# Kernel optimization log

Measured on AMD Instinct MI355X. Metric: run time of the kernel, lower is better.

The kernel has to match this reference:

```python
import jax, jax.numpy as jnp
import numpy as np

TOPK_FRAC = 0.125
RMS_EPS = 1e-6


def setup_inputs() -> dict:
    key = jax.random.key(0)
    ks = jax.random.split(key, 8)
    B, S, D, DH = 8, 8192, 1024, 64
    x = jax.random.normal(ks[0], (B, S, D), dtype=jnp.float32)
    importance = jax.random.normal(ks[1], (B, S), dtype=jnp.float32)
    w_scale = 1.0 / np.sqrt(D)
    W_q = jax.random.normal(ks[2], (2 * DH, D), dtype=jnp.float32) * w_scale
    W_kv = jax.random.normal(ks[3], (3 * DH, D), dtype=jnp.float32) * w_scale
    lam_logit = jnp.float32(-0.5)
    rms_weight = jnp.ones((DH,), dtype=jnp.float32)
    merge_gate = jnp.float32(0.8)
    W_out = jax.random.normal(ks[4], (D, DH), dtype=jnp.float32) * (1.0 / np.sqrt(DH))
    b_out = jnp.zeros((D,), dtype=jnp.float32)
    return {"x": x, "importance": importance, "W_q": W_q, "W_kv": W_kv,
            "lam_logit": lam_logit, "rms_weight": rms_weight,
            "merge_gate": merge_gate, "W_out": W_out, "b_out": b_out}


def reference(x, importance, W_q, W_kv, lam_logit, rms_weight, merge_gate, W_out, b_out):
    B, S, D = x.shape
    dh = rms_weight.shape[0]
    K = max(1, int(TOPK_FRAC * S))
    # SGRSelector: top-K query positions per batch by importance
    _, top_idx = jax.lax.top_k(importance, K)            # [B, K]
    x_sel = jnp.take_along_axis(x, top_idx[:, :, None], axis=1)  # [B, K, D]
    # FusedProjectionSplit: two fused GEMMs
    q = jnp.einsum('bkd,ed->bke', x_sel, W_q)            # [B, K, 2*dh]
    kv = jnp.einsum('bsd,ed->bse', x, W_kv)              # [B, S, 3*dh]
    Q1, Q2 = q[..., :dh], q[..., dh:]
    K1, K2, V = kv[..., :dh], kv[..., dh:2 * dh], kv[..., 2 * dh:]
    scale = 1.0 / jnp.sqrt(jnp.float32(dh))
    # dual-stream differential attention (fp32, like the kernel)
    s1 = jnp.einsum('bke,bse->bks', Q1, K1) * scale
    s2 = jnp.einsum('bke,bse->bks', Q2, K2) * scale
    A1 = jax.nn.softmax(s1, axis=-1)
    A2 = jax.nn.softmax(s2, axis=-1)
    lam = jax.nn.sigmoid(lam_logit)
    attn = jnp.einsum('bks,bse->bke', A1, V) - lam * jnp.einsum('bks,bse->bke', A2, V)  # [B,K,dh]
    # RMSNorm(d_head)
    rms = jnp.sqrt(jnp.mean(attn * attn, axis=-1, keepdims=True) + RMS_EPS)
    h = attn / rms * rms_weight
    # out_proj: d_head -> d_model
    y = jnp.einsum('bke,de->bkd', h, W_out) + b_out      # [B, K, D]
    # gated merge back into the sequence at selected positions
    merged = merge_gate * y + (1.0 - merge_gate) * x_sel
    out = x.at[jnp.arange(B)[:, None], top_idx].set(merged)
    return out
```

## Files before the change

kernel.cpp:

```cpp
#include <hip/hip_runtime.h>

typedef unsigned int u32;
typedef unsigned short u16;
typedef float f32x4_t  __attribute__((ext_vector_type(4)));
typedef float f32x16_t __attribute__((ext_vector_type(16)));
typedef u32   u32x4_t  __attribute__((ext_vector_type(4)));
typedef __bf16 bf16x8_t __attribute__((ext_vector_type(8)));
typedef __bf16 bf16x2_t __attribute__((ext_vector_type(2)));

#define B_   8
#define S_   8192
#define D_   1024
#define KSEL 1024

#define OFF_WQ   0ul
#define OFF_WKV  (256ul<<10)
#define OFF_WO   (640ul<<10)
#define OFF_TIDX (768ul<<10)
#define OFF_K1   (1ul<<20)
#define OFF_K2   (OFF_K1 + (8ul<<20))
#define OFF_V    (OFF_K2 + (8ul<<20))
#define OFF_Q1   (OFF_V  + (8ul<<20))
#define OFF_Q2   (OFF_Q1 + (1ul<<20))
#define OFF_PST  (OFF_Q2 + (1ul<<20))

#define PREC 2304

static __device__ __forceinline__ u16 f2bf(float f){
  return __builtin_bit_cast(u16, (__bf16)f);
}
static __device__ __forceinline__ float bf2f(u16 v){
  u32 u = ((u32)v)<<16; return __builtin_bit_cast(float, u);
}
static __device__ __forceinline__ u32 pkbf(float a, float b){
  bf16x2_t v; v[0] = (__bf16)a; v[1] = (__bf16)b;
  return __builtin_bit_cast(u32, v);
}
static __device__ __forceinline__ f32x16_t zero16(){
  f32x16_t z;
  #pragma unroll
  for (int i=0;i<16;i++) z[i]=0.f;
  return z;
}
static __device__ __forceinline__ bf16x8_t bc8(u32x4_t v){ return __builtin_bit_cast(bf16x8_t, v); }
static __device__ __forceinline__ f32x16_t mfma32(bf16x8_t a, bf16x8_t b, f32x16_t c){
  return __builtin_amdgcn_mfma_f32_32x32x16_bf16(a,b,c,0,0,0);
}
static __device__ __forceinline__ f32x4_t mfma16(bf16x8_t a, bf16x8_t b, f32x4_t c){
  return __builtin_amdgcn_mfma_f32_16x16x32_bf16(a,b,c,0,0,0);
}
static __device__ __forceinline__ void gl_lds16(const void* g, void* l){
  __builtin_amdgcn_global_load_lds((const __attribute__((address_space(1))) u32*)g,
                                   (__attribute__((address_space(3))) u32*)l, 16, 0, 0);
}

__global__ __launch_bounds__(256) void preptopk_kernel(const float* __restrict__ wq,
                                                       const float* __restrict__ wkv,
                                                       const float* __restrict__ wo,
                                                       const float* __restrict__ imp,
                                                       u16* owq, u16* owkv, u16* owo,
                                                       int* __restrict__ tidx){
  if (blockIdx.x >= 8){
    const int i = (blockIdx.x-8)*256 + threadIdx.x;
    if (i < 128*1024) owq[i]  = f2bf(wq[i] * 0.125f);
    if (i < 192*1024) owkv[i] = f2bf(wkv[i]);
    if (i < 64*1024)  owo[i]  = f2bf(wo[i]);
    return;
  }
  const int b = blockIdx.x, t = threadIdx.x;
  __shared__ u32 hist[256];
  __shared__ u32 shPrefix;
  __shared__ int shNeed;
  __shared__ u32 cnt, eqc;
  __shared__ int eqlist[256];
  u32 key[32];
  const float* ip = imp + (long)b*S_;
  #pragma unroll
  for (int i=0;i<32;i++){
    u32 u = __builtin_bit_cast(u32, ip[t + 256*i]);
    key[i] = (u & 0x80000000u) ? ~u : (u | 0x80000000u);
  }
  if (t==0){ shPrefix = 0; shNeed = KSEL; cnt = 0; eqc = 0; }
  for (int pass=0; pass<4; ++pass){
    const int shift = 24 - 8*pass;
    __syncthreads();
    hist[t] = 0;
    __syncthreads();
    const u32 pfx = shPrefix;
    #pragma unroll
    for (int i=0;i<32;i++){
      bool act = (pass==0) || ((key[i] >> (shift+8)) == pfx);
      if (act) atomicAdd(&hist[(key[i]>>shift)&255u], 1u);
    }
    __syncthreads();
    if (t==0){
      int need = shNeed; u32 cum = 0; int c;
      for (c=255; c>=0; --c){ u32 h = hist[c]; if (cum + h >= (u32)need) break; cum += h; }
      if (c < 0) c = 0;
      shPrefix = (shPrefix<<8) | (u32)c;
      shNeed = need - (int)cum;
    }
  }
  __syncthreads();
  const u32 T = shPrefix; const int needEq = shNeed;
  #pragma unroll
  for (int i=0;i<32;i++){
    const int s = t + 256*i;
    if (key[i] > T){ u32 p = atomicAdd(&cnt,1u); tidx[b*KSEL + p] = s; }
    else if (key[i] == T){ u32 e = atomicAdd(&eqc,1u); if (e < 256u) eqlist[e] = s; }
  }
  __syncthreads();
  if (t==0){
    int n = (int)eqc; if (n > 256) n = 256;
    const int bpos = (int)cnt;
    for (int j=0;j<needEq && j<n;j++){
      int mi = j;
      for (int k2=j+1;k2<n;k2++) if (eqlist[k2] < eqlist[mi]) mi = k2;
      int tmp = eqlist[j]; eqlist[j]=eqlist[mi]; eqlist[mi]=tmp;
      tidx[b*KSEL + bpos + j] = eqlist[j];
    }
  }
}

__global__ __launch_bounds__(256,2) void kvq_kernel(const float* __restrict__ x,
                                                    const u16* __restrict__ wkv,
                                                    const u16* __restrict__ wq,
                                                    const int* __restrict__ tidx,
                                                    u16* __restrict__ K1, u16* __restrict__ K2, u16* __restrict__ V,
                                                    u16* __restrict__ Q1, u16* __restrict__ Q2,
                                                    float* __restrict__ out){
  __shared__ __align__(16) char smem[81920];
  const int tid = threadIdx.x;
  const int w = tid>>6, lane = tid&63, lo4 = lane&15, hi = lane>>4;

  if (blockIdx.x < 512){
    char* lA0 = smem;
    char* lB0 = smem + 32768;
    const long row0 = (long)blockIdx.x * 128;
    const int srow8 = tid>>4;
    const int cseg  = tid&15;
    const float* xp = x   + (row0 + srow8)*1024 + cseg*4;
    float*       op = out + (row0 + srow8)*1024 + cseg*4;
    f32x4_t acc[12][2];
    #pragma unroll
    for (int i=0;i<12;i++){ acc[i][0]=(f32x4_t){0,0,0,0}; acc[i][1]=(f32x4_t){0,0,0,0}; }
    f32x4_t f[8];

    auto LOADX = [&](int k0){
      #pragma unroll
      for (int i=0;i<8;i++) f[i] = *(const f32x4_t*)(xp + k0 + i*16*1024);
    };
    auto STORE_WRITE = [&](int k0, int buf){
      #pragma unroll
      for (int i=0;i<8;i++){
        *(f32x4_t*)(op + k0 + i*16*1024) = f[i];
        const u32 row = (u32)(srow8 + i*16);
        u32 byte = row*128u + (u32)cseg*8u;
        byte ^= (row&7u)<<4;
        uint2 p; p.x = pkbf(f[i][0], f[i][1]); p.y = pkbf(f[i][2], f[i][3]);
        *(uint2*)(lA0 + buf*16384 + byte) = p;
      }
    };
    auto STAGEB = [&](int buf, int k0){
      #pragma unroll
      for (int ii=0; ii<6; ++ii){
        const int inst = w*6 + ii;
        const u32 L = (u32)inst*1024u + (u32)lane*16u;
        const u32 n = L>>7, off = L&127u;
        const char* src = (const char*)wkv + (size_t)n*2048 + (size_t)k0*2 + (off ^ ((n&7u)<<4));
        gl_lds16(src, lB0 + buf*24576 + (size_t)inst*1024);
      }
    };

    LOADX(0); STAGEB(0, 0); STORE_WRITE(0, 0);
    __syncthreads();

    for (int t=0; t<16; ++t){
      const int cur = t&1, nxt = cur^1;
      if (t < 15){ LOADX((t+1)*64); STAGEB(nxt, (t+1)*64); }
      #pragma unroll
      for (int kk=0;kk<2;kk++){
        bf16x8_t xf[2];
        #pragma unroll
        for (int ns=0;ns<2;ns++){
          const int s = w*32 + ns*16 + lo4;
          u32 byte = ((u32)s<<7) + ((u32)kk<<6) + ((u32)hi<<4); byte ^= ((u32)(s&7))<<4;
          xf[ns] = *(const bf16x8_t*)(lA0 + cur*16384 + byte);
        }
        #pragma unroll
        for (int ms=0;ms<12;ms++){
          const int e = ms*16 + lo4;
          u32 byte = ((u32)e<<7) + ((u32)kk<<6) + ((u32)hi<<4); byte ^= ((u32)(e&7))<<4;
          const bf16x8_t wf = *(const bf16x8_t*)(lB0 + cur*24576 + byte);
          acc[ms][0] = mfma16(wf, xf[0], acc[ms][0]);
          acc[ms][1] = mfma16(wf, xf[1], acc[ms][1]);
        }
      }
      if (t < 15){ STORE_WRITE((t+1)*64, nxt); }
      __syncthreads();
    }

    #pragma unroll
    for (int ms=0;ms<12;ms++){
      const int e0 = ms*16 + 4*hi;
      const int arr = e0>>6, eh = e0&63;
      u16* basep = arr==0 ? K1 : (arr==1 ? K2 : V);
      #pragma unroll
      for (int ns=0;ns<2;ns++){
        const long srow = row0 + w*32 + ns*16 + lo4;
        ushort4 v;
        v.x = f2bf(acc[ms][ns][0]); v.y = f2bf(acc[ms][ns][1]);
        v.z = f2bf(acc[ms][ns][2]); v.w = f2bf(acc[ms][ns][3]);
        *(ushort4*)(basep + srow*64 + eh) = v;
      }
    }
  } else {
    u16* lW   = (u16*)smem;
    u16* lX   = (u16*)(smem + 16384);
    int* rows = (int*)(smem + 20480);
    const int bq = blockIdx.x - 512;
    const int b = bq >> 5, q0 = (bq & 31) * 32;
    if (tid < 32) rows[tid] = tidx[b*KSEL + q0 + tid];
    __syncthreads();
    const int sq = tid>>3, qt8 = tid&7;
    const float* xp = x + ((long)b*S_ + rows[sq])*1024 + qt8*8;
    f32x4_t acc[2][2];
    #pragma unroll
    for (int i=0;i<2;i++){ acc[i][0]=(f32x4_t){0,0,0,0}; acc[i][1]=(f32x4_t){0,0,0,0}; }

    for (int k0=0;k0<1024;k0+=64){
      __syncthreads();
      f32x4_t f0 = *(const f32x4_t*)(xp + k0);
      f32x4_t f1 = *(const f32x4_t*)(xp + k0 + 4);
      {
        const u32 byte = ((u32)sq<<7) + ((u32)(qt8 ^ (sq&7))<<4);
        *(u32x4_t*)((char*)lX + byte) =
          (u32x4_t){pkbf(f0[0],f0[1]), pkbf(f0[2],f0[3]), pkbf(f1[0],f1[1]), pkbf(f1[2],f1[3])};
      }
      #pragma unroll
      for (int ii=0; ii<4; ++ii){
        const int inst = w*4 + ii;
        const u32 L = (u32)inst*1024u + (u32)lane*16u;
        const u32 n = L>>7, off = L&127u;
        const char* src = (const char*)wq + (size_t)n*2048 + (size_t)k0*2 + (off ^ ((n&7u)<<4));
        gl_lds16(src, (char*)lW + (size_t)inst*1024);
      }
      __syncthreads();
      #pragma unroll
      for (int kk=0;kk<2;kk++){
        bf16x8_t xf[2];
        #pragma unroll
        for (int ns=0;ns<2;ns++){
          const int s = ns*16 + lo4;
          u32 byte = ((u32)s<<7) + ((u32)kk<<6) + ((u32)hi<<4); byte ^= ((u32)(s&7))<<4;
          xf[ns] = *(const bf16x8_t*)((const char*)lX + byte);
        }
        #pragma unroll
        for (int ms=0;ms<2;ms++){
          const int e = w*32 + ms*16 + lo4;
          u32 byte = ((u32)e<<7) + ((u32)kk<<6) + ((u32)hi<<4); byte ^= ((u32)(e&7))<<4;
          const bf16x8_t wf = *(const bf16x8_t*)((const char*)lW + byte);
          acc[ms][0] = mfma16(wf, xf[0], acc[ms][0]);
          acc[ms][1] = mfma16(wf, xf[1], acc[ms][1]);
        }
      }
    }
    #pragma unroll
    for (int ms=0;ms<2;ms++){
      const int e0 = w*32 + ms*16 + 4*hi;
      const int arr = e0>>6, eh = e0&63;
      u16* basep = arr ? Q2 : Q1;
      #pragma unroll
      for (int ns=0;ns<2;ns++){
        const int qg = q0 + ns*16 + lo4;
        ushort4 v;
        v.x = f2bf(acc[ms][ns][0]); v.y = f2bf(acc[ms][ns][1]);
        v.z = f2bf(acc[ms][ns][2]); v.w = f2bf(acc[ms][ns][3]);
        *(ushort4*)(basep + ((long)b*KSEL + qg)*64 + eh) = v;
      }
    }
  }
}

__global__ __launch_bounds__(256,2) void attn_kernel(
    const u16* __restrict__ Q1g, const u16* __restrict__ Q2g,
    const u16* __restrict__ K1g, const u16* __restrict__ K2g,
    const u16* __restrict__ Vg,  u16* __restrict__ pst)
{
  __shared__ __align__(16) u16 lK1[64*64];
  __shared__ __align__(16) u16 lK2[64*64];
  __shared__ __align__(16) u16 lVT[64*64];
  const int tid = threadIdx.x;
  const int w = tid>>6, lane = tid&63;
  const int lo5 = lane&31, hi = lane>>5;
  const int b  = blockIdx.x>>6;
  const int qt = (blockIdx.x>>3)&7;
  const int c  = blockIdx.x&7;
  const int qw = qt*4 + w;
  const int qg = qw*32 + lo5;

  u32x4_t qf[2][4];
  {
    const u16* q1p = Q1g + ((long)b*KSEL + qg)*64;
    const u16* q2p = Q2g + ((long)b*KSEL + qg)*64;
    #pragma unroll
    for (int ks=0;ks<4;ks++){
      qf[0][ks] = *(const u32x4_t*)(q1p + ks*16 + hi*8);
      qf[1][ks] = *(const u32x4_t*)(q2p + ks*16 + hi*8);
    }
  }
  f32x16_t O00 = zero16(), O01 = zero16(), O10 = zero16(), O11 = zero16();
  float m0v = -INFINITY, m1v = -INFINITY, l0v = 0.f, l1v = 0.f;
  const int vkey = tid&63, vdg = tid>>6;

  for (int it=0; it<16; ++it){
    const int s0 = c*1024 + it*64;
    __syncthreads();
    #pragma unroll
    for (int ii=0; ii<2; ++ii){
      const int inst = w*2 + ii;
      const u32 L = (u32)inst*1024u + (u32)lane*16u;
      const u32 r = L>>7;
      const u32 so = (r<<7) | ((L&127u) ^ ((r&7u)<<4));
      const long gb = ((long)(b*S_ + s0))*128;
      gl_lds16((const char*)K1g + gb + so, (char*)lK1 + (size_t)inst*1024);
      gl_lds16((const char*)K2g + gb + so, (char*)lK2 + (size_t)inst*1024);
    }
    {
      const u16* vp = Vg + ((long)(b*S_ + s0 + vkey))*64 + vdg*16;
      const u32x4_t va = *(const u32x4_t*)(vp);
      const u32x4_t vb = *(const u32x4_t*)(vp + 8);
      #pragma unroll
      for (int j=0;j<16;j++){
        const u32 word = (j<8) ? va[(j>>1)&3] : vb[(j>>1)&3];
        const u16 val = (u16)((j&1) ? (word>>16) : (word & 0xffffu));
        const int d = vdg*16 + j;
        u32 byte = ((u32)d<<7) + ((u32)vkey<<1);
        byte ^= ((u32)(d&7))<<4;
        *(u16*)((char*)lVT + byte) = val;
      }
    }
    __syncthreads();
    #pragma unroll
    for (int h=0; h<2; ++h){
      const u16* lK = h ? lK2 : lK1;
      f32x16_t sc0 = zero16(), sc1 = zero16();
      #pragma unroll
      for (int ks=0; ks<4; ++ks){
        u32 byteA = (((u32)lo5)<<7) + ((u32)ks<<5) + ((u32)hi<<4);
        byteA ^= ((u32)(lo5&7))<<4;
        const bf16x8_t kf0 = *(const bf16x8_t*)((const char*)lK + byteA);
        const bf16x8_t kf1 = *(const bf16x8_t*)((const char*)lK + (byteA + 4096));
        sc0 = mfma32(kf0, bc8(qf[h][ks]), sc0);
        sc1 = mfma32(kf1, bc8(qf[h][ks]), sc1);
      }
      const float mref = h ? m1v : m0v;
      float tmax = mref;
      #pragma unroll
      for (int i=0;i<16;i++){ tmax = fmaxf(tmax, sc0[i]); tmax = fmaxf(tmax, sc1[i]); }
      tmax = fmaxf(tmax, __shfl_xor(tmax, 32, 64));
      const float mnew = tmax;
      const float ce = __expf(mref - mnew);
      float lsum = 0.f;
      #pragma unroll
      for (int i=0;i<16;i++){
        sc0[i] = __expf(sc0[i]-mnew); lsum += sc0[i];
        sc1[i] = __expf(sc1[i]-mnew); lsum += sc1[i];
      }
      lsum += __shfl_xor(lsum, 32, 64);
      if (h==0){ l0v = l0v*ce + lsum; m0v = mnew; } else { l1v = l1v*ce + lsum; m1v = mnew; }
      f32x16_t &Oa = h ? O10 : O00;
      f32x16_t &Ob = h ? O11 : O01;
      #pragma unroll
      for (int i=0;i<16;i++){ Oa[i] *= ce; Ob[i] *= ce; }
      #pragma unroll
      for (int kb=0; kb<2; ++kb){
        const f32x16_t &s = kb ? sc1 : sc0;
        u32 pk[8], sx[8];
        #pragma unroll
        for (int i=0;i<8;i++) pk[i] = pkbf(s[2*i], s[2*i+1]);
        #pragma unroll
        for (int i=0;i<8;i++) sx[i] = (u32)__shfl_xor((int)pk[i], 32, 64);
        #pragma unroll
        for (int dd=0; dd<2; ++dd){
          const u32 w0 = hi ? sx[4*dd+2] : pk[4*dd];
          const u32 w1 = hi ? sx[4*dd+3] : pk[4*dd+1];
          const u32 w2 = hi ? pk[4*dd+2] : sx[4*dd];
          const u32 w3 = hi ? pk[4*dd+3] : sx[4*dd+1];
          const bf16x8_t pf = bc8((u32x4_t){w0,w1,w2,w3});
          const int ksG = kb*2 + dd;
          u32 byteV = (((u32)lo5)<<7) + ((u32)ksG<<5) + ((u32)hi<<4);
          byteV ^= ((u32)(lo5&7))<<4;
          const bf16x8_t vf0 = *(const bf16x8_t*)((const char*)lVT + byteV);
          const bf16x8_t vf1 = *(const bf16x8_t*)((const char*)lVT + (byteV + 4096));
          Oa = mfma32(vf0, pf, Oa);
          Ob = mfma32(vf1, pf, Ob);
        }
      }
    }
  }
  const long rec = (((long)b*32 + qw)*8 + c)*2;
  u16* p0 = pst + rec*PREC;
  u16* p1 = p0 + PREC;
  #pragma unroll
  for (int r2=0;r2<16;r2++){
    p0[(   r2)*64 + lane] = f2bf(O00[r2]);
    p0[(16+r2)*64 + lane] = f2bf(O01[r2]);
    p1[(   r2)*64 + lane] = f2bf(O10[r2]);
    p1[(16+r2)*64 + lane] = f2bf(O11[r2]);
  }
  ((float*)(p0+2048))[lane] = m0v; ((float*)(p0+2176))[lane] = l0v;
  ((float*)(p1+2048))[lane] = m1v; ((float*)(p1+2176))[lane] = l1v;
}

__global__ __launch_bounds__(64,1) void combine_kernel(
    const u16* __restrict__ pst, const int* __restrict__ tidx,
    const float* __restrict__ x, const float* __restrict__ rmsw,
    const float* __restrict__ lamp, const float* __restrict__ gatep,
    const u16* __restrict__ wo, const float* __restrict__ bo,
    float* __restrict__ out)
{
  const int lane = threadIdx.x, lo5 = lane&31, hi = lane>>5;
  const int sb = blockIdx.x & 3;
  const int qw = (blockIdx.x>>2) & 31;
  const int b  = blockIdx.x >> 7;
  const float lam = 1.f/(1.f + __expf(-lamp[0]));
  const float g = gatep[0];
  const long rec0 = ((long)b*32 + qw)*16;
  float att[2][16];
  #pragma unroll
  for (int h=0; h<2; ++h){
    const u16* ph = pst + (rec0 + h)*PREC;
    float mc[8], lc[8];
    float mm = -INFINITY;
    #pragma unroll
    for (int cc=0;cc<8;cc++){
      const u16* pc = ph + (size_t)cc*2*PREC;
      mc[cc] = ((const float*)(pc+2048))[lane];
      lc[cc] = ((const float*)(pc+2176))[lane];
      mm = fmaxf(mm, mc[cc]);
    }
    float ef[8]; float L = 0.f;
    #pragma unroll
    for (int cc=0;cc<8;cc++){ ef[cc] = __expf(mc[cc]-mm); L += lc[cc]*ef[cc]; }
    const float invL = 1.f/L;
    #pragma unroll
    for (int dB=0; dB<2; ++dB){
      #pragma unroll
      for (int r=0;r<16;r++){
        float o = 0.f;
        #pragma unroll
        for (int cc=0;cc<8;cc++)
          o += ef[cc]*bf2f(ph[(size_t)cc*2*PREC + (dB*16+r)*64 + lane]);
        o *= invL;
        if (h==0) att[dB][r] = o; else att[dB][r] -= lam*o;
      }
    }
  }
  float ss = 0.f;
  #pragma unroll
  for (int dB=0;dB<2;dB++)
    #pragma unroll
    for (int r=0;r<16;r++) ss += att[dB][r]*att[dB][r];
  ss += __shfl_xor(ss, 32, 64);
  const float inv = rsqrtf(ss*(1.0f/64.0f) + 1e-6f);
  #pragma unroll
  for (int dB=0;dB<2;dB++){
    #pragma unroll
    for (int rq=0;rq<4;rq++){
      const f32x4_t wv = *(const f32x4_t*)(rmsw + dB*32 + 8*rq + 4*hi);
      #pragma unroll
      for (int j=0;j<4;j++) att[dB][4*rq+j] *= inv*wv[j];
    }
  }
  bf16x8_t hf[4];
  #pragma unroll
  for (int dB=0;dB<2;dB++){
    u32 pk[8], sx[8];
    #pragma unroll
    for (int i=0;i<8;i++) pk[i] = pkbf(att[dB][2*i], att[dB][2*i+1]);
    #pragma unroll
    for (int i=0;i<8;i++) sx[i] = (u32)__shfl_xor((int)pk[i], 32, 64);
    #pragma unroll
    for (int dd=0; dd<2; ++dd){
      const u32 w0 = hi ? sx[4*dd+2] : pk[4*dd];
      const u32 w1 = hi ? sx[4*dd+3] : pk[4*dd+1];
      const u32 w2 = hi ? pk[4*dd+2] : sx[4*dd];
      const u32 w3 = hi ? pk[4*dd+3] : sx[4*dd+1];
      hf[dB*2+dd] = bc8((u32x4_t){w0,w1,w2,w3});
    }
  }
  const int srow = tidx[b*KSEL + qw*32 + lo5];
  const float* xr  = x   + ((long)b*S_ + srow)*1024;
  float*       orr = out + ((long)b*S_ + srow)*1024;
  for (int st=sb*8; st<sb*8+8; ++st){
    f32x16_t acc = zero16();
    #pragma unroll
    for (int ks=0;ks<4;ks++){
      const u32x4_t wq4 = *(const u32x4_t*)(wo + ((long)(st*32 + lo5))*64 + ks*16 + hi*8);
      acc = mfma32(bc8(wq4), hf[ks], acc);
    }
    #pragma unroll
    for (int rq=0;rq<4;rq++){
      const int d0 = st*32 + 8*rq + 4*hi;
      const f32x4_t bo4 = *(const f32x4_t*)(bo + d0);
      const f32x4_t xv  = *(const f32x4_t*)(xr + d0);
      f32x4_t mg;
      #pragma unroll
      for (int j=0;j<4;j++){
        const float y = acc[4*rq+j] + bo4[j];
        mg[j] = g*y + (1.f-g)*xv[j];
      }
      *(f32x4_t*)(orr + d0) = mg;
    }
  }
}

extern "C" void kernel_launch(void* const* d_in, const int* in_sizes, int n_in,
                              void* d_out, int out_size, void* d_ws, size_t ws_size,
                              hipStream_t stream) {
  (void)in_sizes; (void)n_in; (void)out_size; (void)ws_size;
  const float* x    = (const float*)d_in[0];
  const float* imp  = (const float*)d_in[1];
  const float* wq   = (const float*)d_in[2];
  const float* wkv  = (const float*)d_in[3];
  const float* lamp = (const float*)d_in[4];
  const float* rmsw = (const float*)d_in[5];
  const float* gate = (const float*)d_in[6];
  const float* wo   = (const float*)d_in[7];
  const float* bo   = (const float*)d_in[8];
  float* out = (float*)d_out;
  char* ws = (char*)d_ws;
  u16* Wq   = (u16*)(ws + OFF_WQ);
  u16* Wkv  = (u16*)(ws + OFF_WKV);
  u16* Wo   = (u16*)(ws + OFF_WO);
  int* Tidx = (int*)(ws + OFF_TIDX);
  u16* K1   = (u16*)(ws + OFF_K1);
  u16* K2   = (u16*)(ws + OFF_K2);
  u16* V    = (u16*)(ws + OFF_V);
  u16* Q1   = (u16*)(ws + OFF_Q1);
  u16* Q2   = (u16*)(ws + OFF_Q2);
  u16* Pst  = (u16*)(ws + OFF_PST);

  preptopk_kernel<<<776, 256, 0, stream>>>(wq, wkv, wo, imp, Wq, Wkv, Wo, Tidx);
  kvq_kernel<<<768, 256, 0, stream>>>(x, Wkv, Wq, Tidx, K1, K2, V, Q1, Q2, out);
  attn_kernel<<<512, 256, 0, stream>>>(Q1, Q2, K1, K2, V, Pst);
  combine_kernel<<<1024, 64, 0, stream>>>(Pst, Tidx, x, rmsw, lamp, gate, Wo, bo, out);
}
```

Before: 272.3 us.

## Fuse combine into attention via last-block atomic counter; lazy rescale; parallel top-k scan

Removes the separate combine kernel: each attention block writes its partial state, increments a per-(batch, query-tile) counter, and the last of the eight chunk blocks performs the merge, RMSNorm and output projection for its tile. The online softmax now rescales only when the running max grows by more than 8, skipping most exp/multiply work on the accumulators. The top-k histogram cut search is replaced by a parallel suffix scan instead of a serial loop in thread 0. The fused epilogue runs on only one block per tile with a serial 32-step output loop, which may create a tail, and the counter relies on threadfence ordering.

```diff
diff --git a/kernel.cpp b/kernel.cpp
--- a/kernel.cpp
+++ b/kernel.cpp
@@ -17,6 +17,7 @@
 #define OFF_WKV  (256ul<<10)
 #define OFF_WO   (640ul<<10)
 #define OFF_TIDX (768ul<<10)
+#define OFF_CNT  (800ul<<10)
 #define OFF_K1   (1ul<<20)
 #define OFF_K2   (OFF_K1 + (8ul<<20))
 #define OFF_V    (OFF_K2 + (8ul<<20))
@@ -59,9 +60,11 @@
                                                        const float* __restrict__ wo,
                                                        const float* __restrict__ imp,
                                                        u16* owq, u16* owkv, u16* owo,
-                                                       int* __restrict__ tidx){
+                                                       int* __restrict__ tidx,
+                                                       int* __restrict__ cnt){
   if (blockIdx.x >= 8){
     const int i = (blockIdx.x-8)*256 + threadIdx.x;
+    if (blockIdx.x == 8 && threadIdx.x < 64) cnt[threadIdx.x] = 0;
     if (i < 128*1024) owq[i]  = f2bf(wq[i] * 0.125f);
     if (i < 192*1024) owkv[i] = f2bf(wkv[i]);
     if (i < 64*1024)  owo[i]  = f2bf(wo[i]);
@@ -69,9 +72,10 @@
   }
   const int b = blockIdx.x, t = threadIdx.x;
   __shared__ u32 hist[256];
+  __shared__ u32 sscan[256];
   __shared__ u32 shPrefix;
   __shared__ int shNeed;
-  __shared__ u32 cnt, eqc;
+  __shared__ u32 cnt2, eqc;
   __shared__ int eqlist[256];
   u32 key[32];
   const float* ip = imp + (long)b*S_;
@@ -80,25 +84,34 @@
     u32 u = __builtin_bit_cast(u32, ip[t + 256*i]);
     key[i] = (u & 0x80000000u) ? ~u : (u | 0x80000000u);
   }
-  if (t==0){ shPrefix = 0; shNeed = KSEL; cnt = 0; eqc = 0; }
+  if (t==0){ shPrefix = 0; shNeed = KSEL; cnt2 = 0; eqc = 0; }
   for (int pass=0; pass<4; ++pass){
     const int shift = 24 - 8*pass;
     __syncthreads();
     hist[t] = 0;
     __syncthreads();
     const u32 pfx = shPrefix;
+    const int need = shNeed;
     #pragma unroll
     for (int i=0;i<32;i++){
       bool act = (pass==0) || ((key[i] >> (shift+8)) == pfx);
       if (act) atomicAdd(&hist[(key[i]>>shift)&255u], 1u);
     }
     __syncthreads();
-    if (t==0){
-      int need = shNeed; u32 cum = 0; int c;
-      for (c=255; c>=0; --c){ u32 h = hist[c]; if (cum + h >= (u32)need) break; cum += h; }
-      if (c < 0) c = 0;
-      shPrefix = (shPrefix<<8) | (u32)c;
-      shNeed = need - (int)cum;
+    sscan[t] = hist[t];
+    __syncthreads();
+    for (int off=1; off<256; off<<=1){
+      const u32 v = (t+off < 256) ? sscan[t+off] : 0u;
+      __syncthreads();
+      sscan[t] += v;
+      __syncthreads();
+    }
+    const u32 un = (u32)need;
+    const u32 s_t  = sscan[t];
+    const u32 s_t1 = (t<255) ? sscan[t+1] : 0u;
+    if (s_t >= un && s_t1 < un){
+      shPrefix = (pfx<<8) | (u32)t;
+      shNeed = need - (int)s_t1;
     }
   }
   __syncthreads();
@@ -106,13 +119,13 @@
   #pragma unroll
   for (int i=0;i<32;i++){
     const int s = t + 256*i;
-    if (key[i] > T){ u32 p = atomicAdd(&cnt,1u); tidx[b*KSEL + p] = s; }
+    if (key[i] > T){ u32 p = atomicAdd(&cnt2,1u); tidx[b*KSEL + p] = s; }
     else if (key[i] == T){ u32 e = atomicAdd(&eqc,1u); if (e < 256u) eqlist[e] = s; }
   }
   __syncthreads();
   if (t==0){
     int n = (int)eqc; if (n > 256) n = 256;
-    const int bpos = (int)cnt;
+    const int bpos = (int)cnt2;
     for (int j=0;j<needEq && j<n;j++){
       int mi = j;
       for (int k2=j+1;k2<n;k2++) if (eqlist[k2] < eqlist[mi]) mi = k2;
@@ -285,11 +298,17 @@
 __global__ __launch_bounds__(256,2) void attn_kernel(
     const u16* __restrict__ Q1g, const u16* __restrict__ Q2g,
     const u16* __restrict__ K1g, const u16* __restrict__ K2g,
-    const u16* __restrict__ Vg,  u16* __restrict__ pst)
+    const u16* __restrict__ Vg,  u16* __restrict__ pst,
+    int* __restrict__ cnt, const int* __restrict__ tidx,
+    const float* __restrict__ x, const float* __restrict__ rmsw,
+    const float* __restrict__ lamp, const float* __restrict__ gatep,
+    const u16* __restrict__ wo, const float* __restrict__ bo,
+    float* __restrict__ out)
 {
   __shared__ __align__(16) u16 lK1[64*64];
   __shared__ __align__(16) u16 lK2[64*64];
   __shared__ __align__(16) u16 lVT[64*64];
+  __shared__ int sOld;
   const int tid = threadIdx.x;
   const int w = tid>>6, lane = tid&63;
   const int lo5 = lane&31, hi = lane>>5;
@@ -355,12 +374,13 @@
         sc1 = mfma32(kf1, bc8(qf[h][ks]), sc1);
       }
       const float mref = h ? m1v : m0v;
-      float tmax = mref;
+      float tmax = -INFINITY;
       #pragma unroll
       for (int i=0;i<16;i++){ tmax = fmaxf(tmax, sc0[i]); tmax = fmaxf(tmax, sc1[i]); }
       tmax = fmaxf(tmax, __shfl_xor(tmax, 32, 64));
-      const float mnew = tmax;
-      const float ce = __expf(mref - mnew);
+      const bool upd = (tmax > mref + 8.f);
+      const float mnew = upd ? tmax : mref;
+      const float ce = upd ? __expf(mref - mnew) : 1.f;
       float lsum = 0.f;
       #pragma unroll
       for (int i=0;i<16;i++){
@@ -368,11 +388,14 @@
         sc1[i] = __expf(sc1[i]-mnew); lsum += sc1[i];
       }
       lsum += __shfl_xor(lsum, 32, 64);
-      if (h==0){ l0v = l0v*ce + lsum; m0v = mnew; } else { l1v = l1v*ce + lsum; m1v = mnew; }
+      if (h==0){ l0v = upd ? l0v*ce + lsum : l0v + lsum; m0v = mnew; }
+      else     { l1v = upd ? l1v*ce + lsum : l1v + lsum; m1v = mnew; }
       f32x16_t &Oa = h ? O10 : O00;
       f32x16_t &Ob = h ? O11 : O01;
-      #pragma unroll
-      for (int i=0;i<16;i++){ Oa[i] *= ce; Ob[i] *= ce; }
+      if (upd){
+        #pragma unroll
+        for (int i=0;i<16;i++){ Oa[i] *= ce; Ob[i] *= ce; }
+      }
       #pragma unroll
       for (int kb=0; kb<2; ++kb){
         const f32x16_t &s = kb ? sc1 : sc0;
@@ -399,31 +422,28 @@
       }
     }
   }
-  const long rec = (((long)b*32 + qw)*8 + c)*2;
-  u16* p0 = pst + rec*PREC;
-  u16* p1 = p0 + PREC;
-  #pragma unroll
-  for (int r2=0;r2<16;r2++){
-    p0[(   r2)*64 + lane] = f2bf(O00[r2]);
-    p0[(16+r2)*64 + lane] = f2bf(O01[r2]);
-    p1[(   r2)*64 + lane] = f2bf(O10[r2]);
-    p1[(16+r2)*64 + lane] = f2bf(O11[r2]);
-  }
-  ((float*)(p0+2048))[lane] = m0v; ((float*)(p0+2176))[lane] = l0v;
-  ((float*)(p1+2048))[lane] = m1v; ((float*)(p1+2176))[lane] = l1v;
-}
-
-__global__ __launch_bounds__(64,1) void combine_kernel(
-    const u16* __restrict__ pst, const int* __restrict__ tidx,
-    const float* __restrict__ x, const float* __restrict__ rmsw,
-    const float* __restrict__ lamp, const float* __restrict__ gatep,
-    const u16* __restrict__ wo, const float* __restrict__ bo,
-    float* __restrict__ out)
-{
-  const int lane = threadIdx.x, lo5 = lane&31, hi = lane>>5;
-  const int sb = blockIdx.x & 3;
-  const int qw = (blockIdx.x>>2) & 31;
-  const int b  = blockIdx.x >> 7;
+  {
+    const long rec = (((long)b*32 + qw)*8 + c)*2;
+    u16* p0 = pst + rec*PREC;
+    u16* p1 = p0 + PREC;
+    #pragma unroll
+    for (int r2=0;r2<16;r2++){
+      p0[(   r2)*64 + lane] = f2bf(O00[r2]);
+      p0[(16+r2)*64 + lane] = f2bf(O01[r2]);
+      p1[(   r2)*64 + lane] = f2bf(O10[r2]);
+      p1[(16+r2)*64 + lane] = f2bf(O11[r2]);
+    }
+    ((float*)(p0+2048))[lane] = m0v; ((float*)(p0+2176))[lane] = l0v;
+    ((float*)(p1+2048))[lane] = m1v; ((float*)(p1+2176))[lane] = l1v;
+  }
+
+  __threadfence();
+  __syncthreads();
+  if (tid==0) sOld = atomicAdd(&cnt[b*8+qt], 1);
+  __syncthreads();
+  if (sOld != 7) return;
+  __threadfence();
+
   const float lam = 1.f/(1.f + __expf(-lamp[0]));
   const float g = gatep[0];
   const long rec0 = ((long)b*32 + qw)*16;
@@ -493,7 +513,7 @@
   const int srow = tidx[b*KSEL + qw*32 + lo5];
   const float* xr  = x   + ((long)b*S_ + srow)*1024;
   float*       orr = out + ((long)b*S_ + srow)*1024;
-  for (int st=sb*8; st<sb*8+8; ++st){
+  for (int st=0; st<32; ++st){
     f32x16_t acc = zero16();
     #pragma unroll
     for (int ks=0;ks<4;ks++){
@@ -535,6 +555,7 @@
   u16* Wkv  = (u16*)(ws + OFF_WKV);
   u16* Wo   = (u16*)(ws + OFF_WO);
   int* Tidx = (int*)(ws + OFF_TIDX);
+  int* Cnt  = (int*)(ws + OFF_CNT);
   u16* K1   = (u16*)(ws + OFF_K1);
   u16* K2   = (u16*)(ws + OFF_K2);
   u16* V    = (u16*)(ws + OFF_V);
@@ -542,8 +563,8 @@
   u16* Q2   = (u16*)(ws + OFF_Q2);
   u16* Pst  = (u16*)(ws + OFF_PST);
 
-  preptopk_kernel<<<776, 256, 0, stream>>>(wq, wkv, wo, imp, Wq, Wkv, Wo, Tidx);
+  preptopk_kernel<<<776, 256, 0, stream>>>(wq, wkv, wo, imp, Wq, Wkv, Wo, Tidx, Cnt);
   kvq_kernel<<<768, 256, 0, stream>>>(x, Wkv, Wq, Tidx, K1, K2, V, Q1, Q2, out);
-  attn_kernel<<<512, 256, 0, stream>>>(Q1, Q2, K1, K2, V, Pst);
-  combine_kernel<<<1024, 64, 0, stream>>>(Pst, Tidx, x, rmsw, lamp, gate, Wo, bo, out);
-}
+  attn_kernel<<<512, 256, 0, stream>>>(Q1, Q2, K1, K2, V, Pst, Cnt, Tidx,
+                                       x, rmsw, lamp, gate, Wo, bo, out);
+}
```

New measurement: 412.6 us. +51.5%, slower.
